# Kernel tuning notes

Hardware: AMD Instinct MI355X
Metric: run time of the kernel (lower is better)

Reference implementation:

```python
import jax, jax.numpy as jnp
import numpy as np

B, T = 8, 32
DSENS, DA = 512, 32
DS = DE = DIM = 128  # dim_structure = dim_encoded_sensory = memory dim


def l2norm(x, eps=1e-12):
    return x / jnp.maximum(jnp.linalg.norm(x, axis=-1, keepdims=True), eps)


def mlp3(x, W1, b1, W2, b2, W3, b3):
    h = jax.nn.relu(x @ W1 + b1)
    h = jax.nn.relu(h @ W2 + b2)
    return h @ W3 + b3


def mse(a, b):
    return jnp.mean((a - b) ** 2)


def assoc_scan(x, gate, prev):
    # h_t = gate_t * h_{t-1} + x_t with h_0 = prev.  x:[b,t,w], gate:[b,t,1], prev:[b,w]
    x = x.at[:, 0].add(gate[:, 0] * prev)
    def combine(ca, cb):
        ga, xa = ca
        gb, xb = cb
        return ga * gb, xb + gb * xa
    _, h = jax.lax.associative_scan(combine, (gate, x), axis=1)
    return h


def _forward(sensory, actions, enc_w, dec_w, pi_w1, pi_b1, pi_w2, pi_b2, pi_w3, pi_b3,
             rnn_init_hidden, wq, wk, wv, w_hp, m_w1, m_b1, m_w2, m_b2, m_w3, m_b3,
             o_w1, o_b1, o_w2, o_b2, o_w3, o_b3, v_w1, v_b1, v_w2, v_b2, v_w3, v_b3,
             integration_ratio):
    b, t = actions.shape[:2]
    # --- path integration: action MLP -> per-step transition matrices -> sequential RNN scan ---
    trans = mlp3(actions, pi_w1, pi_b1, pi_w2, pi_b2, pi_w3, pi_b3).reshape(b, t, DS, DS)
    h0 = jnp.broadcast_to(l2norm(rnn_init_hidden)[0], (b, DS))
    def step(h, Tm):
        h = l2norm(jax.nn.relu(jnp.einsum('bi,bij->bj', h, Tm)))
        return h, h
    _, hs = jax.lax.scan(step, h0, jnp.moveaxis(trans, 1, 0))
    structural = jnp.moveaxis(hs, 0, 1)                      # [b,t,DS]

    enc = sensory @ enc_w                                    # [b,t,DE]
    meta_p = (m_w1, m_b1, m_w2, m_b2, m_w3, m_b3)

    def retrieve(s, e):
        q = jnp.concatenate([s, e], axis=-1) @ wq            # to_queries
        r = mlp3(q, *meta_p)                                 # meta_memory_mlp (slow copy)
        d = mlp3(r, o_w1, o_b1, o_w2, o_b2, o_w3, o_b3)      # memory_output_decoder
        return d[..., :DS], d[..., DS:]

    dec_gen_s, dec_enc = retrieve(structural, jnp.zeros_like(enc))
    gen_loss = mse(sensory, dec_enc @ dec_w)
    dec_s2, _ = retrieve(jnp.zeros_like(structural), enc)
    relational_loss = 2.0 * mse(dec_s2, structural)          # source computes the identical loss twice
    corr_s, corr_e = retrieve(dec_gen_s, enc)
    sse = jnp.sum((corr_e - enc) ** 2, axis=-1, keepdims=True)
    pred_var = mlp3(jnp.concatenate([corr_s, dec_gen_s, sse], axis=-1),
                    v_w1, v_b1, v_w2, v_b2, v_w3, v_b3)
    inf_s = dec_gen_s + (corr_s - dec_gen_s) * jax.nn.sigmoid(integration_ratio) * pred_var
    consistency_loss = mse(dec_gen_s, inf_s)
    final_s, inf_e = retrieve(inf_s, jnp.zeros_like(enc))
    inf_loss = mse(sensory, inf_e @ dec_w)

    # --- test-time-training memory write: per-sample meta-grads + two assoc scans ---
    joint = jnp.concatenate([final_s, enc], axis=-1)         # [b,t,2*DS]
    keys, values = joint @ wk, joint @ wv                    # [b,t,DIM]
    hp = joint @ w_hp                                        # [b,t,3]
    lr, forget, beta = hp[..., 0], hp[..., 1], hp[..., 2]

    def meta_loss(p, k, v):
        return jnp.mean((mlp3(k, *p) - v) ** 2)
    pb = tuple(jnp.broadcast_to(p, (b,) + p.shape) for p in meta_p)
    grads = jax.vmap(jax.vmap(jax.grad(meta_loss), in_axes=(None, 0, 0)))(pb, keys, values)
    G = jnp.concatenate([g.reshape(b, t, -1) for g in grads], axis=-1)  # [b,t,Wtot]
    W = G.shape[-1]
    p_flat = jnp.broadcast_to(jnp.concatenate([p.ravel() for p in meta_p])[None], (b, W))
    update = assoc_scan(G * lr[..., None], jax.nn.sigmoid(beta)[..., None],
                        jnp.zeros((b, W), G.dtype))          # momentum scan
    acc = assoc_scan(-update, jax.nn.sigmoid(forget)[..., None], p_flat)  # weight-decay scan
    next_state = jnp.concatenate([acc[:, -1], update[:, -1]], axis=-1)    # [b,2W]

    total = gen_loss + relational_loss + consistency_loss + inf_loss
    return jnp.concatenate([jnp.reshape(total, (1,)), next_state.ravel()])


def setup_inputs() -> dict:
    key = jax.random.key(0)
    ks = iter(jax.random.split(key, 48))
    def rn(shape, s=1.0):
        return jax.random.normal(next(ks), shape, dtype=jnp.float32) * s
    def lin(fi, fo):
        return rn((fi, fo), 1.0 / np.sqrt(fi))
    z = lambda n: jnp.zeros((n,), jnp.float32)
    return {
        "sensory": rn((B, T, DSENS)),
        "actions": rn((B, T, DA)),
        "enc_w": lin(DSENS, DE), "dec_w": lin(DE, DSENS),
        "pi_w1": lin(DA, 4 * DA), "pi_b1": z(4 * DA),
        "pi_w2": lin(4 * DA, 4 * DA), "pi_b2": z(4 * DA),
        "pi_w3": lin(4 * DA, DS * DS), "pi_b3": z(DS * DS),
        "rnn_init_hidden": rn((1, DS), 0.01),
        "wq": lin(DS + DE, DIM), "wk": lin(DS + DE, DIM), "wv": lin(DS + DE, DIM),
        "w_hp": lin(DS + DE, 3),
        "m_w1": lin(DIM, 2 * DIM), "m_b1": z(2 * DIM),
        "m_w2": lin(2 * DIM, 2 * DIM), "m_b2": z(2 * DIM),
        "m_w3": lin(2 * DIM, DIM), "m_b3": z(DIM),
        "o_w1": lin(DIM, 2 * DIM), "o_b1": z(2 * DIM),
        "o_w2": lin(2 * DIM, 2 * DIM), "o_b2": z(2 * DIM),
        "o_w3": lin(2 * DIM, DS + DE), "o_b3": z(DS + DE),
        "v_w1": lin(2 * DS + 1, 2 * DS), "v_b1": z(2 * DS),
        "v_w2": lin(2 * DS, 2 * DS), "v_b2": z(2 * DS),
        "v_w3": lin(2 * DS, DS), "v_b3": z(DS),
        "integration_ratio": jnp.zeros((), jnp.float32),
    }


def reference(sensory, actions, enc_w, dec_w, pi_w1, pi_b1, pi_w2, pi_b2, pi_w3, pi_b3,
              rnn_init_hidden, wq, wk, wv, w_hp, m_w1, m_b1, m_w2, m_b2, m_w3, m_b3,
              o_w1, o_b1, o_w2, o_b2, o_w3, o_b3, v_w1, v_b1, v_w2, v_b2, v_w3, v_b3,
              integration_ratio):
    return _forward(sensory, actions, enc_w, dec_w, pi_w1, pi_b1, pi_w2, pi_b2, pi_w3, pi_b3,
                    rnn_init_hidden, wq, wk, wv, w_hp, m_w1, m_b1, m_w2, m_b2, m_w3, m_b3,
                    o_w1, o_b1, o_w2, o_b2, o_w3, o_b3, v_w1, v_b1, v_w2, v_b2, v_w3, v_b3,
                    integration_ratio)
```

## Files before the change

kernel.cpp:

```cpp
#include <hip/hip_runtime.h>
#include <cstdint>
#include <cstddef>

#define DEV __device__ __forceinline__

constexpr size_t W_TOT = 131712;
constexpr size_t OFF_W1 = 0;
constexpr size_t OFF_B1 = 32768;
constexpr size_t OFF_W2 = 33024;
constexpr size_t OFF_B2 = 98560;
constexpr size_t OFF_W3 = 98816;
constexpr size_t OFF_B3 = 131584;

constexpr int OPS = 272;

constexpr size_t P_LOSS = 0;
constexpr size_t P_WA   = 1024;
constexpr size_t P_WU   = 1280;
constexpr size_t P_FT   = 1536;
constexpr size_t P_HP   = 2048;
constexpr size_t P_H2PI = 4096;
constexpr size_t P_ENC  = P_H2PI + 32768;
constexpr size_t P_DGS  = P_ENC + 32768;
constexpr size_t P_INF  = P_DGS + 32768;
constexpr size_t P_KEYS = P_INF + 32768;
constexpr size_t P_VALS = P_KEYS + 32768;
constexpr size_t P_D3   = P_VALS + 32768;
constexpr size_t P_H1   = P_D3 + 32768;
constexpr size_t P_H2   = P_H1 + 65536;
constexpr size_t P_D1   = P_H2 + 65536;
constexpr size_t P_D2   = P_D1 + 65536;
constexpr size_t P_STRUCT = P_D2 + 65536;
constexpr size_t P_TRANS  = P_STRUCT + 32768;

DEV float sigm(float x) { return 1.f / (1.f + expf(-x)); }

DEV float wgsum256(float v, float* red) {
#pragma unroll
  for (int s = 32; s > 0; s >>= 1) v += __shfl_xor(v, s);
  if ((threadIdx.x & 63) == 0) red[threadIdx.x >> 6] = v;
  __syncthreads();
  const float t = red[0] + red[1] + red[2] + red[3];
  __syncthreads();
  return t;
}

template<int K, int OUT, int ROWS>
DEV void denseW(const float* __restrict__ W, const float* __restrict__ bias,
                const float* in, int ips, float* out, int ops, int relu,
                float* scr)
{
  constexpr int OUTG = OUT / 4;
  constexpr int HALF = OUTG / 2;
  constexpr int TPS  = HALF;
  constexpr int NSEG = 256 / TPS;
  constexpr int KS   = K / NSEG;
  constexpr int NG   = KS / 8;
  static_assert(KS % 8 == 0 && NG >= 1, "bad shape");
  const int tid = (int)threadIdx.x;
  const int c   = tid & (TPS - 1);
  const int seg = tid / TPS;
  const int k0  = seg * KS;
  const float4* W4 = reinterpret_cast<const float4*>(W);
  float4 a0[8], b0[8], a1[8], b1[8];
  float acc[ROWS][8];
#pragma unroll
  for (int r = 0; r < ROWS; ++r)
#pragma unroll
    for (int x = 0; x < 8; ++x) acc[r][x] = 0.f;
#pragma unroll
  for (int u = 0; u < 8; ++u) {
    a0[u] = W4[(size_t)(k0 + u) * OUTG + c];
    b0[u] = W4[(size_t)(k0 + u) * OUTG + c + HALF];
  }
#pragma unroll
  for (int t = 1; t <= NG; ++t) {
    if (t < NG) {
#pragma unroll
      for (int u = 0; u < 8; ++u) {
        a1[u] = W4[(size_t)(k0 + t * 8 + u) * OUTG + c];
        b1[u] = W4[(size_t)(k0 + t * 8 + u) * OUTG + c + HALF];
      }
    }
#pragma unroll
    for (int u = 0; u < 8; ++u) {
      const int kk = k0 + (t - 1) * 8 + u;
#pragma unroll
      for (int r = 0; r < ROWS; ++r) {
        const float x = in[r * ips + kk];
        acc[r][0] = fmaf(x, a0[u].x, acc[r][0]);
        acc[r][1] = fmaf(x, a0[u].y, acc[r][1]);
        acc[r][2] = fmaf(x, a0[u].z, acc[r][2]);
        acc[r][3] = fmaf(x, a0[u].w, acc[r][3]);
        acc[r][4] = fmaf(x, b0[u].x, acc[r][4]);
        acc[r][5] = fmaf(x, b0[u].y, acc[r][5]);
        acc[r][6] = fmaf(x, b0[u].z, acc[r][6]);
        acc[r][7] = fmaf(x, b0[u].w, acc[r][7]);
      }
    }
    if (t < NG) {
#pragma unroll
      for (int u = 0; u < 8; ++u) { a0[u] = a1[u]; b0[u] = b1[u]; }
    }
  }
  float4* s4 = reinterpret_cast<float4*>(scr);
#pragma unroll
  for (int r = 0; r < ROWS; ++r) {
    s4[(seg * ROWS + r) * OUTG + c] =
        make_float4(acc[r][0], acc[r][1], acc[r][2], acc[r][3]);
    s4[(seg * ROWS + r) * OUTG + c + HALF] =
        make_float4(acc[r][4], acc[r][5], acc[r][6], acc[r][7]);
  }
  __syncthreads();
  for (int idx = tid; idx < OUT * ROWS; idx += 256) {
    const int r = idx / OUT, j = idx % OUT;
    float v = (bias ? bias[j] : 0.f);
#pragma unroll
    for (int s = 0; s < NSEG; ++s) v += scr[(s * ROWS + r) * OUT + j];
    if (relu) v = fmaxf(v, 0.f);
    out[r * ops + j] = v;
  }
  __syncthreads();
}

__global__ __launch_bounds__(128) void k_pi_h2(
    const float* __restrict__ actions,
    const float* __restrict__ w1, const float* __restrict__ b1,
    const float* __restrict__ w2, const float* __restrict__ b2,
    float* __restrict__ h2out)
{
  const int row = blockIdx.x;
  const int j = threadIdx.x;
  __shared__ float a[32];
  __shared__ float h1[128];
  if (j < 32) a[j] = actions[row * 32 + j];
  __syncthreads();
  float acc = b1[j];
#pragma unroll
  for (int i = 0; i < 32; ++i) acc = fmaf(a[i], w1[i * 128 + j], acc);
  h1[j] = fmaxf(acc, 0.f);
  __syncthreads();
  float acc2 = b2[j];
#pragma unroll 8
  for (int i = 0; i < 128; ++i) acc2 = fmaf(h1[i], w2[i * 128 + j], acc2);
  h2out[row * 128 + j] = fmaxf(acc2, 0.f);
}

__global__ __launch_bounds__(256) void k_pi_trans(
    const float* __restrict__ h2,
    const float* __restrict__ w3, const float* __restrict__ b3,
    float* __restrict__ trans)
{
  const int col = blockIdx.x * 256 + threadIdx.x;
  const int r0 = blockIdx.y * 32;
  __shared__ float h2s[32][128];
  for (int idx = threadIdx.x; idx < 32 * 128; idx += 256)
    h2s[idx >> 7][idx & 127] = h2[(size_t)(r0 + (idx >> 7)) * 128 + (idx & 127)];
  __syncthreads();
  float acc[32];
#pragma unroll
  for (int r = 0; r < 32; ++r) acc[r] = 0.f;
  float w0[8], w1[8];
#pragma unroll
  for (int c = 0; c < 8; ++c) w0[c] = w3[(size_t)c * 16384 + col];
#pragma unroll
  for (int i = 8; i <= 128; i += 8) {
    if (i < 128) {
#pragma unroll
      for (int c = 0; c < 8; ++c) w1[c] = w3[(size_t)(i + c) * 16384 + col];
    }
#pragma unroll
    for (int r = 0; r < 32; ++r) {
      float s = acc[r];
#pragma unroll
      for (int c = 0; c < 8; ++c) s = fmaf(h2s[r][i - 8 + c], w0[c], s);
      acc[r] = s;
    }
    if (i < 128) {
#pragma unroll
      for (int c = 0; c < 8; ++c) w0[c] = w1[c];
    }
  }
  const float bv = b3[col];
#pragma unroll
  for (int r = 0; r < 32; ++r)
    trans[(size_t)(r0 + r) * 16384 + col] = acc[r] + bv;
}

__global__ __launch_bounds__(1024) void k_rnn(
    const float* __restrict__ trans, const float* __restrict__ rinit,
    float* __restrict__ structural)
{
  const int b = blockIdx.x;
  const int tid = threadIdx.x;
  const int j = tid & 127, seg = tid >> 7;
  __shared__ float h[128];
  __shared__ float part[8][128];
  __shared__ float ssq;
  if (tid < 128) h[tid] = rinit[tid];
  __syncthreads();
  if (tid < 64) {
    float v = h[tid] * h[tid] + h[tid + 64] * h[tid + 64];
#pragma unroll
    for (int s = 32; s > 0; s >>= 1) v += __shfl_xor(v, s);
    if (tid == 0) ssq = v;
  }
  __syncthreads();
  if (tid < 128) h[tid] /= fmaxf(sqrtf(ssq), 1e-12f);
  __syncthreads();

  float cur[16], nxt[16];
  {
    const float* T0 = trans + ((size_t)(b * 32) << 14);
#pragma unroll
    for (int k = 0; k < 16; ++k) cur[k] = T0[(size_t)(seg * 16 + k) * 128 + j];
  }
  for (int t = 0; t < 32; ++t) {
    if (t < 31) {
      const float* Tn = trans + ((size_t)(b * 32 + t + 1) << 14);
#pragma unroll
      for (int k = 0; k < 16; ++k) nxt[k] = Tn[(size_t)(seg * 16 + k) * 128 + j];
    }
    float acc = 0.f;
#pragma unroll
    for (int k = 0; k < 16; ++k) acc = fmaf(h[seg * 16 + k], cur[k], acc);
    part[seg][j] = acc;
    __syncthreads();
    if (tid < 128) {
      float r = part[0][j];
#pragma unroll
      for (int s = 1; s < 8; ++s) r += part[s][j];
      part[0][j] = fmaxf(r, 0.f);
    }
    __syncthreads();
    if (tid < 64) {
      float v = part[0][tid] * part[0][tid] + part[0][tid + 64] * part[0][tid + 64];
#pragma unroll
      for (int s = 32; s > 0; s >>= 1) v += __shfl_xor(v, s);
      if (tid == 0) ssq = v;
    }
    __syncthreads();
    if (tid < 128) {
      const float nv = part[0][j] / fmaxf(sqrtf(ssq), 1e-12f);
      h[j] = nv;
      structural[(size_t)(b * 32 + t) * 128 + j] = nv;
    }
    __syncthreads();
    if (t < 31) {
#pragma unroll
      for (int k = 0; k < 16; ++k) cur[k] = nxt[k];
    }
  }
}

__global__ __launch_bounds__(256) void kA(
    const float* __restrict__ sensory, const float* __restrict__ structural_,
    const float* __restrict__ enc_w, const float* __restrict__ wq,
    const float* __restrict__ dec_w,
    const float* __restrict__ mw1, const float* __restrict__ mb1,
    const float* __restrict__ mw2, const float* __restrict__ mb2,
    const float* __restrict__ mw3, const float* __restrict__ mb3,
    const float* __restrict__ ow1, const float* __restrict__ ob1,
    const float* __restrict__ ow2, const float* __restrict__ ob2,
    const float* __restrict__ ow3, const float* __restrict__ ob3,
    float* __restrict__ ws_enc, float* __restrict__ ws_dgs,
    float* __restrict__ lossPart)
{
  const int g = blockIdx.x, tid = threadIdx.x;
  __shared__ float sens[512], sRow[128], eRow[128];
  __shared__ float actA[2 * OPS], actB[2 * OPS];
  __shared__ float4 scr4buf[1024];
  __shared__ float red[4];
  float* scr = reinterpret_cast<float*>(scr4buf);

  for (int i = tid; i < 512; i += 256) sens[i] = sensory[(size_t)g * 512 + i];
  if (tid < 128) sRow[tid] = structural_[(size_t)g * 128 + tid];
  __syncthreads();

  denseW<512, 128, 1>(enc_w, nullptr, sens, 0, eRow, 0, 0, scr);
  if (tid < 128) ws_enc[(size_t)g * 128 + tid] = eRow[tid];

  denseW<128, 128, 1>(wq, nullptr, sRow, 0, actA, 0, 0, scr);
  denseW<128, 128, 1>(wq + 128 * 128, nullptr, eRow, 0, actA + OPS, 0, 0, scr);
  denseW<128, 256, 2>(mw1, mb1, actA, OPS, actB, OPS, 1, scr);
  denseW<256, 256, 2>(mw2, mb2, actB, OPS, actA, OPS, 1, scr);
  denseW<256, 128, 2>(mw3, mb3, actA, OPS, actB, OPS, 0, scr);
  denseW<128, 256, 2>(ow1, ob1, actB, OPS, actA, OPS, 1, scr);
  denseW<256, 256, 2>(ow2, ob2, actA, OPS, actB, OPS, 1, scr);
  denseW<256, 256, 2>(ow3, ob3, actB, OPS, actA, OPS, 0, scr);
  float lrel = 0.f;
  if (tid < 128) {
    ws_dgs[(size_t)g * 128 + tid] = actA[tid];
    const float d = actA[OPS + tid] - sRow[tid];
    lrel = d * d;
  }
  const float relT = wgsum256(lrel, red);
  if (tid == 0) lossPart[256 + g] = relT;
  denseW<128, 512, 1>(dec_w, nullptr, &actA[128], 0, actB, 0, 0, scr);
  {
    float ls = 0.f;
    for (int j2 = tid; j2 < 512; j2 += 256) {
      const float d = actB[j2] - sens[j2];
      ls = fmaf(d, d, ls);
    }
    const float genT = wgsum256(ls, red);
    if (tid == 0) lossPart[g] = genT;
  }
}

__global__ __launch_bounds__(256) void kB(
    const float* __restrict__ ws_enc, const float* __restrict__ ws_dgs,
    const float* __restrict__ wq,
    const float* __restrict__ mw1, const float* __restrict__ mb1,
    const float* __restrict__ mw2, const float* __restrict__ mb2,
    const float* __restrict__ mw3, const float* __restrict__ mb3,
    const float* __restrict__ ow1, const float* __restrict__ ob1,
    const float* __restrict__ ow2, const float* __restrict__ ob2,
    const float* __restrict__ ow3, const float* __restrict__ ob3,
    const float* __restrict__ vw1, const float* __restrict__ vb1,
    const float* __restrict__ vw2, const float* __restrict__ vb2,
    const float* __restrict__ vw3, const float* __restrict__ vb3,
    const float* __restrict__ ir,
    float* __restrict__ ws_inf, float* __restrict__ lossPart)
{
  const int g = blockIdx.x, tid = threadIdx.x;
  __shared__ float eRow[128], dgsRow[128], cRow[128];
  __shared__ float cbuf[256];
  __shared__ float actA[2 * OPS], actB[2 * OPS];
  __shared__ float4 scr4buf[1024];
  __shared__ float red[4];
  float* scr = reinterpret_cast<float*>(scr4buf);

  if (tid < 128) eRow[tid] = ws_enc[(size_t)g * 128 + tid];
  else dgsRow[tid - 128] = ws_dgs[(size_t)g * 128 + (tid - 128)];
  __syncthreads();

  cbuf[tid] = (tid < 128) ? dgsRow[tid] : eRow[tid - 128];
  __syncthreads();
  denseW<256, 128, 1>(wq, nullptr, cbuf, 0, actA, 0, 0, scr);
  denseW<128, 256, 1>(mw1, mb1, actA, 0, actB, 0, 1, scr);
  denseW<256, 256, 1>(mw2, mb2, actB, 0, actA, 0, 1, scr);
  denseW<256, 128, 1>(mw3, mb3, actA, 0, actB, 0, 0, scr);
  denseW<128, 256, 1>(ow1, ob1, actB, 0, actA, 0, 1, scr);
  denseW<256, 256, 1>(ow2, ob2, actA, 0, actB, 0, 1, scr);
  denseW<256, 256, 1>(ow3, ob3, actB, 0, actA, 0, 0, scr);
  float ls = 0.f;
  if (tid < 128) {
    cRow[tid] = actA[tid];
    const float d = actA[128 + tid] - eRow[tid];
    ls = d * d;
  }
  const float sseV = wgsum256(ls, red);

  cbuf[tid] = (tid < 128) ? cRow[tid] : dgsRow[tid - 128];
  __syncthreads();
  denseW<256, 256, 1>(vw1, vb1, cbuf, 0, actB, 0, 0, scr);
  actB[tid] = fmaxf(actB[tid] + sseV * vw1[(size_t)256 * 256 + tid], 0.f);
  __syncthreads();
  denseW<256, 256, 1>(vw2, vb2, actB, 0, actA, 0, 1, scr);
  denseW<256, 128, 1>(vw3, vb3, actA, 0, actB, 0, 0, scr);
  const float sig = sigm(ir[0]);
  float lc = 0.f;
  if (tid < 128) {
    const float diff = (cRow[tid] - dgsRow[tid]) * sig * actB[tid];
    ws_inf[(size_t)g * 128 + tid] = dgsRow[tid] + diff;
    lc = diff * diff;
  }
  const float consT = wgsum256(lc, red);
  if (tid == 0) lossPart[512 + g] = consT;
}

__global__ __launch_bounds__(256) void kC(
    const float* __restrict__ sensory,
    const float* __restrict__ ws_enc, const float* __restrict__ ws_inf,
    const float* __restrict__ wq, const float* __restrict__ dec_w,
    const float* __restrict__ mw1, const float* __restrict__ mb1,
    const float* __restrict__ mw2, const float* __restrict__ mb2,
    const float* __restrict__ mw3, const float* __restrict__ mb3,
    const float* __restrict__ ow1, const float* __restrict__ ob1,
    const float* __restrict__ ow2, const float* __restrict__ ob2,
    const float* __restrict__ ow3, const float* __restrict__ ob3,
    const float* __restrict__ wk, const float* __restrict__ wv,
    const float* __restrict__ w_hp,
    float* __restrict__ gKeys, float* __restrict__ gVals,
    float* __restrict__ gHp, float* __restrict__ lossPart)
{
  const int g = blockIdx.x, tid = threadIdx.x;
  __shared__ float sens[512], eRow[128], infRow[128];
  __shared__ float cbuf[256];
  __shared__ float actA[2 * OPS], actB[2 * OPS];
  __shared__ float4 scr4buf[1024];
  __shared__ float red[4];
  float* scr = reinterpret_cast<float*>(scr4buf);

  for (int i = tid; i < 512; i += 256) sens[i] = sensory[(size_t)g * 512 + i];
  if (tid < 128) eRow[tid] = ws_enc[(size_t)g * 128 + tid];
  else infRow[tid - 128] = ws_inf[(size_t)g * 128 + (tid - 128)];
  __syncthreads();

  denseW<128, 128, 1>(wq, nullptr, infRow, 0, actA, 0, 0, scr);
  denseW<128, 256, 1>(mw1, mb1, actA, 0, actB, 0, 1, scr);
  denseW<256, 256, 1>(mw2, mb2, actB, 0, actA, 0, 1, scr);
  denseW<256, 128, 1>(mw3, mb3, actA, 0, actB, 0, 0, scr);
  denseW<128, 256, 1>(ow1, ob1, actB, 0, actA, 0, 1, scr);
  denseW<256, 256, 1>(ow2, ob2, actA, 0, actB, 0, 1, scr);
  denseW<256, 256, 1>(ow3, ob3, actB, 0, actA, 0, 0, scr);
  denseW<128, 512, 1>(dec_w, nullptr, &actA[128], 0, actB, 0, 0, scr);
  {
    float ls = 0.f;
    for (int j2 = tid; j2 < 512; j2 += 256) {
      const float d = actB[j2] - sens[j2];
      ls = fmaf(d, d, ls);
    }
    const float infT = wgsum256(ls, red);
    if (tid == 0) lossPart[768 + g] = infT;
  }
  __syncthreads();

  cbuf[tid] = (tid < 128) ? actA[tid] : eRow[tid - 128];
  __syncthreads();
  denseW<256, 128, 1>(wk, nullptr, cbuf, 0, gKeys + (size_t)g * 128, 0, 0, scr);
  denseW<256, 128, 1>(wv, nullptr, cbuf, 0, gVals + (size_t)g * 128, 0, 0, scr);
  const int c = tid >> 6, l = tid & 63;
  float acc = 0.f;
  if (c < 3) {
    for (int i = l; i < 256; i += 64)
      acc = fmaf(cbuf[i], w_hp[i * 3 + c], acc);
  }
#pragma unroll
  for (int s = 32; s > 0; s >>= 1) acc += __shfl_xor(acc, s);
  if (c < 3 && l == 0) gHp[(size_t)g * 4 + c] = acc;
}

__global__ __launch_bounds__(256) void kD(
    const float* __restrict__ gKeys, const float* __restrict__ gVals,
    const float* __restrict__ gHp,
    const float* __restrict__ mw1, const float* __restrict__ mb1,
    const float* __restrict__ mw2, const float* __restrict__ mb2,
    const float* __restrict__ mw3, const float* __restrict__ mb3,
    float* __restrict__ ws_h1, float* __restrict__ ws_h2,
    float* __restrict__ ws_d1, float* __restrict__ ws_d2, float* __restrict__ ws_d3,
    float* __restrict__ wA, float* __restrict__ wU, float* __restrict__ Ft)
{
  const int tid = threadIdx.x;
  __shared__ float kRow[128], vRow[128];
  __shared__ float actA[256], actB[256], d3R[128], d2R[256];
  __shared__ float4 scr4buf[1024];
  __shared__ float lr[256], sf[256], sb[256];
  float* scr = reinterpret_cast<float*>(scr4buf);
  if (blockIdx.x == 256) {
    lr[tid] = gHp[(size_t)tid * 4 + 0];
    sf[tid] = sigm(gHp[(size_t)tid * 4 + 1]);
    sb[tid] = sigm(gHp[(size_t)tid * 4 + 2]);
    __syncthreads();
    if (tid < 8) {
      const int b = tid;
      float cB = 1.f, cF = 1.f, Bv = 1.f;
      wU[b * 32 + 31] = lr[b * 32 + 31];
      wA[b * 32 + 31] = lr[b * 32 + 31];
      for (int t = 30; t >= 0; --t) {
        cB = sb[b * 32 + t + 1] * cB;
        cF = sf[b * 32 + t + 1] * cF;
        Bv = cF + sb[b * 32 + t + 1] * Bv;
        wU[b * 32 + t] = lr[b * 32 + t] * cB;
        wA[b * 32 + t] = lr[b * 32 + t] * Bv;
      }
      float ft = 1.f;
      for (int t = 0; t < 32; ++t) ft *= sf[b * 32 + t];
      Ft[b] = ft;
    }
    return;
  }
  const int g = blockIdx.x;
  if (tid < 128) kRow[tid] = gKeys[(size_t)g * 128 + tid];
  else vRow[tid - 128] = gVals[(size_t)g * 128 + (tid - 128)];
  __syncthreads();
  denseW<128, 256, 1>(mw1, mb1, kRow, 0, actA, 0, 1, scr);
  ws_h1[(size_t)g * 256 + tid] = actA[tid];
  denseW<256, 256, 1>(mw2, mb2, actA, 0, actB, 0, 1, scr);
  ws_h2[(size_t)g * 256 + tid] = actB[tid];
  denseW<256, 128, 1>(mw3, mb3, actB, 0, d3R, 0, 0, scr);
  if (tid < 128) {
    const float d = (d3R[tid] - vRow[tid]) * (2.f / 128.f);
    d3R[tid] = d;
    ws_d3[(size_t)g * 128 + tid] = d;
  }
  __syncthreads();
  {
    const int j = tid;
    float acc = 0.f;
    for (int jc = 0; jc < 128; jc += 4) {
      const float4 w = *reinterpret_cast<const float4*>(&mw3[(size_t)j * 128 + jc]);
      acc = fmaf(w.x, d3R[jc + 0], acc);
      acc = fmaf(w.y, d3R[jc + 1], acc);
      acc = fmaf(w.z, d3R[jc + 2], acc);
      acc = fmaf(w.w, d3R[jc + 3], acc);
    }
    const float v = (actB[j] > 0.f) ? acc : 0.f;
    d2R[j] = v;
    ws_d2[(size_t)g * 256 + j] = v;
  }
  __syncthreads();
  {
    const int j = tid;
    float acc = 0.f;
    for (int jc = 0; jc < 256; jc += 4) {
      const float4 w = *reinterpret_cast<const float4*>(&mw2[(size_t)j * 256 + jc]);
      acc = fmaf(w.x, d2R[jc + 0], acc);
      acc = fmaf(w.y, d2R[jc + 1], acc);
      acc = fmaf(w.z, d2R[jc + 2], acc);
      acc = fmaf(w.w, d2R[jc + 3], acc);
    }
    ws_d1[(size_t)g * 256 + j] = (actA[j] > 0.f) ? acc : 0.f;
  }
}

DEV void outer_body(const float* __restrict__ L, int Lld,
                    const float* __restrict__ D, int Dld,
                    const float* __restrict__ P,
                    const float* __restrict__ wA, const float* __restrict__ wU,
                    const float* __restrict__ Ftot,
                    float* __restrict__ out, size_t regionOff, int J,
                    int b, int i0, float* __restrict__ wAk, float* __restrict__ wUk)
{
  const int tid = threadIdx.x;
  for (int idx = tid; idx < 1024; idx += 256) {
    const int t = idx >> 5, ii = idx & 31;
    const float kv = L[(size_t)(b * 32 + t) * Lld + i0 + ii];
    wAk[t * 33 + ii] = wA[b * 32 + t] * kv;
    wUk[t * 33 + ii] = wU[b * 32 + t] * kv;
  }
  __syncthreads();
  const int j = (J == 256) ? tid : (tid & 127);
  const int g2 = (J == 256) ? 0 : (tid >> 7);
  const int span = (J == 256) ? 32 : 16;
  const int iBeg = g2 * span;
  float dv[32];
#pragma unroll
  for (int t = 0; t < 32; ++t) dv[t] = D[(size_t)(b * 32 + t) * Dld + j];
  const float ft = Ftot[b];
  float* ob = out + 1 + (size_t)b * (2 * W_TOT);
  for (int ii = iBeg; ii < iBeg + span; ++ii) {
    float aA = 0.f, aU = 0.f;
#pragma unroll
    for (int t = 0; t < 32; ++t) {
      aA = fmaf(wAk[t * 33 + ii], dv[t], aA);
      aU = fmaf(wUk[t * 33 + ii], dv[t], aU);
    }
    const int i = i0 + ii;
    const size_t w = regionOff + (size_t)i * J + j;
    ob[w] = ft * P[(size_t)i * J + j] - aA;
    ob[W_TOT + w] = aU;
  }
}

__global__ __launch_bounds__(256) void kW(
    const float* __restrict__ keys, const float* __restrict__ h1,
    const float* __restrict__ h2, const float* __restrict__ d1,
    const float* __restrict__ d2, const float* __restrict__ d3,
    const float* __restrict__ mw1, const float* __restrict__ mb1,
    const float* __restrict__ mw2, const float* __restrict__ mb2,
    const float* __restrict__ mw3, const float* __restrict__ mb3,
    const float* __restrict__ wA, const float* __restrict__ wU,
    const float* __restrict__ Ft, const float* __restrict__ lossPart,
    float* __restrict__ out)
{
  __shared__ float wAk[32 * 33], wUk[32 * 33];
  __shared__ float red[4];
  const int bid = blockIdx.x;
  const int tid = threadIdx.x;
  if (bid < 32) {
    outer_body(keys, 128, d1, 256, mw1, wA, wU, Ft, out, OFF_W1, 256,
               bid >> 2, (bid & 3) * 32, wAk, wUk);
  } else if (bid < 96) {
    const int x = bid - 32;
    outer_body(h1, 256, d2, 256, mw2, wA, wU, Ft, out, OFF_W2, 256,
               x >> 3, (x & 7) * 32, wAk, wUk);
  } else if (bid < 160) {
    const int x = bid - 96;
    outer_body(h2, 256, d3, 128, mw3, wA, wU, Ft, out, OFF_W3, 128,
               x >> 3, (x & 7) * 32, wAk, wUk);
  } else if (bid < 168) {
    const int b = bid - 160;
    const float ft = Ft[b];
    float* ob = out + 1 + (size_t)b * (2 * W_TOT);
    for (int idx = tid; idx < 640; idx += 256) {
      const float* D; int ld, j; size_t off; float pv;
      if (idx < 256)      { D = d1; ld = 256; j = idx;       off = OFF_B1; pv = mb1[j]; }
      else if (idx < 512) { D = d2; ld = 256; j = idx - 256; off = OFF_B2; pv = mb2[j]; }
      else                { D = d3; ld = 128; j = idx - 512; off = OFF_B3; pv = mb3[j]; }
      float aA = 0.f, aU = 0.f;
#pragma unroll
      for (int t = 0; t < 32; ++t) {
        const float dv = D[(size_t)(b * 32 + t) * ld + j];
        aA = fmaf(wA[b * 32 + t], dv, aA);
        aU = fmaf(wU[b * 32 + t], dv, aU);
      }
      ob[off + j] = ft * pv - aA;
      ob[W_TOT + off + j] = aU;
    }
  } else {
    const int c = tid >> 6, l = tid & 63;
    float v = lossPart[c * 256 + l] + lossPart[c * 256 + 64 + l] +
              lossPart[c * 256 + 128 + l] + lossPart[c * 256 + 192 + l];
#pragma unroll
    for (int s = 32; s > 0; s >>= 1) v += __shfl_xor(v, s);
    if (l == 0) red[c] = v;
    __syncthreads();
    if (tid == 0) {
      const float i1 = 1.f / (256.f * 512.f);
      const float i2 = 1.f / (256.f * 128.f);
      out[0] = red[0] * i1 + 2.f * red[1] * i2 + red[2] * i2 + red[3] * i1;
    }
  }
}

extern "C" void kernel_launch(void* const* d_in, const int* in_sizes, int n_in,
                              void* d_out, int out_size, void* d_ws, size_t ws_size,
                              hipStream_t stream)
{
  const float* sensory = (const float*)d_in[0];
  const float* actions = (const float*)d_in[1];
  const float* enc_w = (const float*)d_in[2];
  const float* dec_w = (const float*)d_in[3];
  const float* pi_w1 = (const float*)d_in[4];
  const float* pi_b1 = (const float*)d_in[5];
  const float* pi_w2 = (const float*)d_in[6];
  const float* pi_b2 = (const float*)d_in[7];
  const float* pi_w3 = (const float*)d_in[8];
  const float* pi_b3 = (const float*)d_in[9];
  const float* rinit = (const float*)d_in[10];
  const float* wq = (const float*)d_in[11];
  const float* wk = (const float*)d_in[12];
  const float* wv = (const float*)d_in[13];
  const float* w_hp = (const float*)d_in[14];
  const float* mw1 = (const float*)d_in[15]; const float* mb1 = (const float*)d_in[16];
  const float* mw2 = (const float*)d_in[17]; const float* mb2 = (const float*)d_in[18];
  const float* mw3 = (const float*)d_in[19]; const float* mb3 = (const float*)d_in[20];
  const float* ow1 = (const float*)d_in[21]; const float* ob1 = (const float*)d_in[22];
  const float* ow2 = (const float*)d_in[23]; const float* ob2 = (const float*)d_in[24];
  const float* ow3 = (const float*)d_in[25]; const float* ob3 = (const float*)d_in[26];
  const float* vw1 = (const float*)d_in[27]; const float* vb1 = (const float*)d_in[28];
  const float* vw2 = (const float*)d_in[29]; const float* vb2 = (const float*)d_in[30];
  const float* vw3 = (const float*)d_in[31]; const float* vb3 = (const float*)d_in[32];
  const float* ir  = (const float*)d_in[33];

  float* ws  = (float*)d_ws;
  float* out = (float*)d_out;

  float* lossP = ws + P_LOSS;
  float* wA = ws + P_WA; float* wU = ws + P_WU; float* Ft = ws + P_FT;
  float* hp = ws + P_HP;
  float* h2pi = ws + P_H2PI;
  float* enc = ws + P_ENC;
  float* dgs = ws + P_DGS;
  float* inf = ws + P_INF;
  float* keys = ws + P_KEYS;
  float* vals = ws + P_VALS;
  float* d3s = ws + P_D3;
  float* h1s = ws + P_H1;
  float* h2s = ws + P_H2;
  float* d1s = ws + P_D1;
  float* d2s = ws + P_D2;
  float* structural = ws + P_STRUCT;
  float* trans = ws + P_TRANS;

  hipLaunchKernelGGL(k_pi_h2, dim3(256), dim3(128), 0, stream,
                     actions, pi_w1, pi_b1, pi_w2, pi_b2, h2pi);
  hipLaunchKernelGGL(k_pi_trans, dim3(64, 8), dim3(256), 0, stream,
                     h2pi, pi_w3, pi_b3, trans);
  hipLaunchKernelGGL(k_rnn, dim3(8), dim3(1024), 0, stream, trans, rinit, structural);
  hipLaunchKernelGGL(kA, dim3(256), dim3(256), 0, stream,
                     sensory, structural, enc_w, wq, dec_w,
                     mw1, mb1, mw2, mb2, mw3, mb3,
                     ow1, ob1, ow2, ob2, ow3, ob3,
                     enc, dgs, lossP);
  hipLaunchKernelGGL(kB, dim3(256), dim3(256), 0, stream,
                     enc, dgs, wq,
                     mw1, mb1, mw2, mb2, mw3, mb3,
                     ow1, ob1, ow2, ob2, ow3, ob3,
                     vw1, vb1, vw2, vb2, vw3, vb3,
                     ir, inf, lossP);
  hipLaunchKernelGGL(kC, dim3(256), dim3(256), 0, stream,
                     sensory, enc, inf, wq, dec_w,
                     mw1, mb1, mw2, mb2, mw3, mb3,
                     ow1, ob1, ow2, ob2, ow3, ob3,
                     wk, wv, w_hp, keys, vals, hp, lossP);
  hipLaunchKernelGGL(kD, dim3(257), dim3(256), 0, stream,
                     keys, vals, hp, mw1, mb1, mw2, mb2, mw3, mb3,
                     h1s, h2s, d1s, d2s, d3s, wA, wU, Ft);
  hipLaunchKernelGGL(kW, dim3(169), dim3(256), 0, stream,
                     keys, h1s, h2s, d1s, d2s, d3s,
                     mw1, mb1, mw2, mb2, mw3, mb3,
                     wA, wU, Ft, lossP, out);
}
```

Before: 193.2 us.

## Run RNN scan with one wavefront per batch using shuffle reductions

The recurrent path-integration kernel drops from 1024 threads to a single 64-lane wavefront per batch. Each lane computes two output columns over the full 128-long dot product, with chunked register prefetch of the transition matrix. The L2 norm uses warp shuffles, which removes the shared-memory partial-sum reduction and most block barriers. In exchange, far fewer threads issue loads for each 64 KB transition matrix, and the next timestep's matrix is no longer prefetched across steps.

```diff
diff --git a/kernel.cpp b/kernel.cpp
--- a/kernel.cpp
+++ b/kernel.cpp
@@ -187,69 +187,66 @@
     trans[(size_t)(r0 + r) * 16384 + col] = acc[r] + bv;
 }
 
-__global__ __launch_bounds__(1024) void k_rnn(
+__global__ __launch_bounds__(64) void k_rnn(
     const float* __restrict__ trans, const float* __restrict__ rinit,
     float* __restrict__ structural)
 {
   const int b = blockIdx.x;
-  const int tid = threadIdx.x;
-  const int j = tid & 127, seg = tid >> 7;
+  const int l = (int)threadIdx.x;
   __shared__ float h[128];
-  __shared__ float part[8][128];
-  __shared__ float ssq;
-  if (tid < 128) h[tid] = rinit[tid];
-  __syncthreads();
-  if (tid < 64) {
-    float v = h[tid] * h[tid] + h[tid + 64] * h[tid + 64];
-#pragma unroll
-    for (int s = 32; s > 0; s >>= 1) v += __shfl_xor(v, s);
-    if (tid == 0) ssq = v;
-  }
-  __syncthreads();
-  if (tid < 128) h[tid] /= fmaxf(sqrtf(ssq), 1e-12f);
-  __syncthreads();
-
-  float cur[16], nxt[16];
   {
-    const float* T0 = trans + ((size_t)(b * 32) << 14);
-#pragma unroll
-    for (int k = 0; k < 16; ++k) cur[k] = T0[(size_t)(seg * 16 + k) * 128 + j];
-  }
+    const float x0 = rinit[l], x1 = rinit[l + 64];
+    float ss = x0 * x0 + x1 * x1;
+#pragma unroll
+    for (int s = 32; s > 0; s >>= 1) ss += __shfl_xor(ss, s);
+    const float iv = 1.f / fmaxf(sqrtf(ss), 1e-12f);
+    h[l] = x0 * iv;
+    h[l + 64] = x1 * iv;
+  }
+  __syncthreads();
+
   for (int t = 0; t < 32; ++t) {
-    if (t < 31) {
-      const float* Tn = trans + ((size_t)(b * 32 + t + 1) << 14);
-#pragma unroll
-      for (int k = 0; k < 16; ++k) nxt[k] = Tn[(size_t)(seg * 16 + k) * 128 + j];
-    }
-    float acc = 0.f;
-#pragma unroll
-    for (int k = 0; k < 16; ++k) acc = fmaf(h[seg * 16 + k], cur[k], acc);
-    part[seg][j] = acc;
+    const float* T = trans + ((size_t)(b * 32 + t) << 14);
+    float a0 = 0.f, a1 = 0.f;
+    float c0[8], c1[8], n0[8], n1[8];
+#pragma unroll
+    for (int u = 0; u < 8; ++u) {
+      c0[u] = T[(size_t)u * 128 + l];
+      c1[u] = T[(size_t)u * 128 + l + 64];
+    }
+#pragma unroll
+    for (int ch = 1; ch <= 16; ++ch) {
+      if (ch < 16) {
+#pragma unroll
+        for (int u = 0; u < 8; ++u) {
+          n0[u] = T[(size_t)(ch * 8 + u) * 128 + l];
+          n1[u] = T[(size_t)(ch * 8 + u) * 128 + l + 64];
+        }
+      }
+#pragma unroll
+      for (int u = 0; u < 8; ++u) {
+        const float hv = h[(ch - 1) * 8 + u];
+        a0 = fmaf(hv, c0[u], a0);
+        a1 = fmaf(hv, c1[u], a1);
+      }
+      if (ch < 16) {
+#pragma unroll
+        for (int u = 0; u < 8; ++u) { c0[u] = n0[u]; c1[u] = n1[u]; }
+      }
+    }
+    a0 = fmaxf(a0, 0.f);
+    a1 = fmaxf(a1, 0.f);
+    float s2 = a0 * a0 + a1 * a1;
+#pragma unroll
+    for (int s = 32; s > 0; s >>= 1) s2 += __shfl_xor(s2, s);
+    const float iv = 1.f / fmaxf(sqrtf(s2), 1e-12f);
+    const float v0 = a0 * iv, v1 = a1 * iv;
     __syncthreads();
-    if (tid < 128) {
-      float r = part[0][j];
-#pragma unroll
-      for (int s = 1; s < 8; ++s) r += part[s][j];
-      part[0][j] = fmaxf(r, 0.f);
-    }
+    h[l] = v0;
+    h[l + 64] = v1;
     __syncthreads();
-    if (tid < 64) {
-      float v = part[0][tid] * part[0][tid] + part[0][tid + 64] * part[0][tid + 64];
-#pragma unroll
-      for (int s = 32; s > 0; s >>= 1) v += __shfl_xor(v, s);
-      if (tid == 0) ssq = v;
-    }
-    __syncthreads();
-    if (tid < 128) {
-      const float nv = part[0][j] / fmaxf(sqrtf(ssq), 1e-12f);
-      h[j] = nv;
-      structural[(size_t)(b * 32 + t) * 128 + j] = nv;
-    }
-    __syncthreads();
-    if (t < 31) {
-#pragma unroll
-      for (int k = 0; k < 16; ++k) cur[k] = nxt[k];
-    }
+    structural[(size_t)(b * 32 + t) * 128 + l] = v0;
+    structural[(size_t)(b * 32 + t) * 128 + l + 64] = v1;
   }
 }
 
@@ -669,7 +666,7 @@
                      actions, pi_w1, pi_b1, pi_w2, pi_b2, h2pi);
   hipLaunchKernelGGL(k_pi_trans, dim3(64, 8), dim3(256), 0, stream,
                      h2pi, pi_w3, pi_b3, trans);
-  hipLaunchKernelGGL(k_rnn, dim3(8), dim3(1024), 0, stream, trans, rinit, structural);
+  hipLaunchKernelGGL(k_rnn, dim3(8), dim3(64), 0, stream, trans, rinit, structural);
   hipLaunchKernelGGL(kA, dim3(256), dim3(256), 0, stream,
                      sensory, structural, enc_w, wq, dec_w,
                      mw1, mb1, mw2, mb2, mw3, mb3,
```

Measured after the change: 351.5 us. 81.9% more time.
